# Optimization experiments

Measured on AMD Instinct MI355X. Metric: run time of the kernel, lower is better.

## Reference

```python
import jax, jax.numpy as jnp
import numpy as np

N = 20000
E = 320000
DIM_IN, DIM_H, DIM_OUT, HEADS = 500, 32, 16, 8
NEG_SLOPE = 0.2


def _glorot(key, shape, fan_in, fan_out):
    s = jnp.sqrt(6.0 / (fan_in + fan_out))
    return jax.random.uniform(key, shape, jnp.float32, -s, s)


def setup_inputs() -> dict:
    key = jax.random.key(0)
    ks = jax.random.split(key, 16)
    x = jax.random.normal(ks[0], (N, DIM_IN), jnp.float32)
    edge_index = jax.random.randint(ks[1], (2, E), 0, N, jnp.int64)
    h1 = HEADS * DIM_H   # 256
    h2 = HEADS * DIM_OUT  # 128
    return {
        "x": x,
        "edge_index": edge_index,
        # layer 1: GATv2Conv(500, 32, heads=8), concat -> 256
        "W1l": _glorot(ks[2], (h1, DIM_IN), DIM_IN, h1),
        "b1l": jnp.zeros((h1,), jnp.float32),
        "W1r": _glorot(ks[3], (h1, DIM_IN), DIM_IN, h1),
        "b1r": jnp.zeros((h1,), jnp.float32),
        "att1": _glorot(ks[4], (HEADS, DIM_H), DIM_H, 1),
        "bias1": jnp.zeros((h1,), jnp.float32),
        # layer 2: GATv2Conv(256, 16, heads=8), concat -> 128
        "W2l": _glorot(ks[5], (h2, h1), h1, h2),
        "b2l": jnp.zeros((h2,), jnp.float32),
        "W2r": _glorot(ks[6], (h2, h1), h1, h2),
        "b2r": jnp.zeros((h2,), jnp.float32),
        "att2": _glorot(ks[7], (HEADS, DIM_OUT), DIM_OUT, 1),
        "bias2": jnp.zeros((h2,), jnp.float32),
    }


def _gatv2_layer(x, Wl, bl, Wr, br, att, bias, src, dst, heads, out_ch):
    n = x.shape[0]
    xl = (x @ Wl.T + bl).reshape(n, heads, out_ch)  # source transform
    xr = (x @ Wr.T + br).reshape(n, heads, out_ch)  # target transform
    e = xl[src] + xr[dst]                            # [E', H, C]
    e = jnp.where(e >= 0, e, NEG_SLOPE * e)          # LeakyReLU(0.2)
    logits = jnp.einsum('ehc,hc->eh', e, att)        # [E', H]
    # segment softmax over incoming edges of each dst node
    m = jax.ops.segment_max(logits, dst, num_segments=n)
    ex = jnp.exp(logits - m[dst])
    denom = jax.ops.segment_sum(ex, dst, num_segments=n)
    alpha = ex / denom[dst]                          # [E', H]
    out = jax.ops.segment_sum(xl[src] * alpha[:, :, None], dst, num_segments=n)
    return out.reshape(n, heads * out_ch) + bias


def reference(x, edge_index, W1l, b1l, W1r, b1r, att1, bias1,
              W2l, b2l, W2r, b2r, att2, bias2):
    n = x.shape[0]
    loop = jnp.arange(n, dtype=edge_index.dtype)
    src = jnp.concatenate([edge_index[0], loop])  # PyG add_self_loops=True
    dst = jnp.concatenate([edge_index[1], loop])
    h = _gatv2_layer(x, W1l, b1l, W1r, b1r, att1, bias1, src, dst, HEADS, DIM_H)
    h = jax.nn.elu(h)  # normalization='none' -> Identity; eval-mode dropout is identity
    h = _gatv2_layer(h, W2l, b2l, W2r, b2r, att2, bias2, src, dst, HEADS, DIM_OUT)
    return jax.nn.log_softmax(h, axis=1)
```

## Files before the change

kernel.cpp:

```cpp
#include <hip/hip_runtime.h>
#include <math.h>

#define DIN   500
#define H1    256
#define H2    128
#define NEG_SLOPE 0.2f

typedef __attribute__((ext_vector_type(8))) short short8;
typedef __attribute__((ext_vector_type(4))) float floatx4;

static __device__ __forceinline__ unsigned short f2bf(float f) {
    union { float f; unsigned int u; } x; x.f = f;
    unsigned int r = x.u + 0x7fffu + ((x.u >> 16) & 1u);
    return (unsigned short)(r >> 16);
}
static __device__ __forceinline__ float bitsf(unsigned int i) {
    union { unsigned int i; float f; } x; x.i = i;
    return x.f;
}
static __device__ __forceinline__ void cvt8(uint4 u, float* o) {
    o[0] = bitsf(u.x << 16); o[1] = bitsf(u.x & 0xffff0000u);
    o[2] = bitsf(u.y << 16); o[3] = bitsf(u.y & 0xffff0000u);
    o[4] = bitsf(u.z << 16); o[5] = bitsf(u.z & 0xffff0000u);
    o[6] = bitsf(u.w << 16); o[7] = bitsf(u.w & 0xffff0000u);
}

template<int SHIFT>
static __device__ __forceinline__ void cast_seg(const float* __restrict__ src,
                                                unsigned short* __restrict__ dst,
                                                int M, int K, long base, long total) {
    if (base >= total) return;
    int row = (int)(base >> SHIFT);
    int c   = (int)(base & ((1 << SHIFT) - 1));
    const float* srow = src + (size_t)row * K;
    unsigned short tmp[8];
    #pragma unroll
    for (int j = 0; j < 8; ++j) {
        int cc = c + j;
        float v = (row < M && cc < K) ? srow[cc] : 0.f;
        tmp[j] = f2bf(v);
    }
    *reinterpret_cast<int4*>(dst + base) = *reinterpret_cast<const int4*>(tmp);
}

__global__ __launch_bounds__(256) void prep(const float* __restrict__ x,
                                            const float* __restrict__ W1l,
                                            const float* __restrict__ W1r,
                                            const float* __restrict__ W2l,
                                            const float* __restrict__ W2r,
                                            unsigned short* __restrict__ xb,
                                            unsigned short* __restrict__ W1b,
                                            unsigned short* __restrict__ W2b,
                                            int* __restrict__ counts,
                                            int N, int Mpad,
                                            int ZB, int XB, int W1B, int W2B) {
    int bid = blockIdx.x;
    int tid = threadIdx.x;
    if (bid < ZB) {
        int i = bid * 256 + tid;
        if (i < N) counts[i] = 1;
        else if (i == N) counts[N] = 0;
        return;
    }
    bid -= ZB;
    if (bid < XB) {
        long base = ((long)bid * 256 + tid) * 8;
        cast_seg<9>(x, xb, N, DIN, base, (long)Mpad * 512);
        return;
    }
    bid -= XB;
    if (bid < W1B) {
        long base = ((long)bid * 256 + tid) * 8;
        cast_seg<9>(W1l, W1b, H1, DIN, base, (long)H1 * 512);
        return;
    }
    bid -= W1B;
    if (bid < W1B) {
        long base = ((long)bid * 256 + tid) * 8;
        cast_seg<9>(W1r, W1b + (size_t)H1 * 512, H1, DIN, base, (long)H1 * 512);
        return;
    }
    bid -= W1B;
    if (bid < W2B) {
        long base = ((long)bid * 256 + tid) * 8;
        cast_seg<8>(W2l, W2b, H2, H1, base, (long)H2 * H1);
        return;
    }
    bid -= W2B;
    {
        long base = ((long)bid * 256 + tid) * 8;
        cast_seg<8>(W2r, W2b + (size_t)H2 * H1, H2, H1, base, (long)H2 * H1);
    }
}


__global__ void count_deg(const int* __restrict__ dst, int E, int* __restrict__ counts) {
    int i = blockIdx.x * blockDim.x + threadIdx.x;
    if (i < E) atomicAdd(&counts[dst[i]], 1);
}

__global__ __launch_bounds__(1024) void scan_all(const int* __restrict__ counts,
                                                 int* __restrict__ excl,
                                                 int* __restrict__ bsum,
                                                 int* __restrict__ done,
                                                 int* __restrict__ offsets,
                                                 int* __restrict__ cursor,
                                                 int n, int total_edges, int nb) {
    __shared__ int s[1024];
    __shared__ int sb[32];
    __shared__ int ticket;
    int tid = threadIdx.x;
    int bid = blockIdx.x;
    int i = bid * 1024 + tid;
    int v = (i < n) ? counts[i] : 0;
    s[tid] = v;
    __syncthreads();
    #pragma unroll
    for (int off = 1; off < 1024; off <<= 1) {
        int t = (tid >= off) ? s[tid - off] : 0;
        __syncthreads();
        s[tid] += t;
        __syncthreads();
    }
    if (i < n) excl[i] = s[tid] - v;
    if (tid == 1023) bsum[bid] = s[1023];
    __syncthreads();
    if (tid == 0) {
        __threadfence();
        ticket = __hip_atomic_fetch_add(done, 1, __ATOMIC_ACQ_REL, __HIP_MEMORY_SCOPE_AGENT);
    }
    __syncthreads();
    if (ticket == nb - 1) {
        __threadfence();
        if (tid == 0) {
            int run = 0;
            for (int j = 0; j < nb; ++j) { int t = bsum[j]; sb[j] = run; run += t; }
        }
        __syncthreads();
        for (int j = tid; j < n; j += 1024) {
            int o = excl[j] + sb[j >> 10];
            offsets[j] = o;
            cursor[j]  = o;
        }
        if (tid == 0) offsets[n] = total_edges;
    }
}

template<int MODE>
static __device__ __forceinline__ void gemm_body(unsigned short* lA, unsigned short* lB,
                                                 const unsigned short* __restrict__ A,
                                                 const unsigned short* __restrict__ W,
                                                 const float* __restrict__ b_lo,
                                                 const float* __restrict__ b_hi,
                                                 int halfN,
                                                 unsigned short* __restrict__ Cb,
                                                 float* __restrict__ Cf,
                                                 int M, int Nc, int K,
                                                 int bm, int bn) {
    int tid  = threadIdx.x;
    int lane = tid & 63;
    int wid  = tid >> 6;
    int wr   = wid >> 1, wc = wid & 1;

    floatx4 acc[4][4] = {};

    int st_r = (lane >> 3);
    int st_p = (lane & 7);

    for (int k0 = 0; k0 < K; k0 += 64) {
        #pragma unroll
        for (int i = 0; i < 4; ++i) {
            int r = i * 32 + wid * 8 + st_r;
            int s = st_p ^ (r & 7);
            const unsigned short* ga = A + (size_t)(bm + r) * K + k0 + s * 8;
            const unsigned short* gb = W + (size_t)(bn + r) * K + k0 + s * 8;
            __builtin_amdgcn_global_load_lds(
                (const __attribute__((address_space(1))) void*)ga,
                (__attribute__((address_space(3))) void*)((char*)lA + i * 4096 + wid * 1024),
                16, 0, 0);
            __builtin_amdgcn_global_load_lds(
                (const __attribute__((address_space(1))) void*)gb,
                (__attribute__((address_space(3))) void*)((char*)lB + i * 4096 + wid * 1024),
                16, 0, 0);
        }
        __syncthreads();

        #pragma unroll
        for (int kk = 0; kk < 2; ++kk) {
            int sbase = kk * 4 + (lane >> 4);
            short8 af[4], bf[4];
            #pragma unroll
            for (int ar = 0; ar < 4; ++ar) {
                int lr = wr * 64 + ar * 16 + (lane & 15);
                af[ar] = *reinterpret_cast<const short8*>(
                    (const char*)lA + lr * 128 + ((sbase ^ (lr & 7)) * 16));
            }
            #pragma unroll
            for (int bc = 0; bc < 4; ++bc) {
                int lc = wc * 64 + bc * 16 + (lane & 15);
                bf[bc] = *reinterpret_cast<const short8*>(
                    (const char*)lB + lc * 128 + ((sbase ^ (lc & 7)) * 16));
            }
            #pragma unroll
            for (int ar = 0; ar < 4; ++ar)
                #pragma unroll
                for (int bc = 0; bc < 4; ++bc)
                    acc[ar][bc] = __builtin_amdgcn_mfma_f32_16x16x32_bf16(
                        af[ar], bf[bc], acc[ar][bc], 0, 0, 0);
        }
        __syncthreads();
    }

    #pragma unroll
    for (int ar = 0; ar < 4; ++ar) {
        #pragma unroll
        for (int bc = 0; bc < 4; ++bc) {
            int col = bn + wc * 64 + bc * 16 + (lane & 15);
            float bv = (col < halfN) ? b_lo[col] : b_hi[col - halfN];
            #pragma unroll
            for (int r = 0; r < 4; ++r) {
                int row = bm + wr * 64 + ar * 16 + (lane >> 4) * 4 + r;
                if (row < M) {
                    float v = acc[ar][bc][r] + bv;
                    if (MODE == 1) {
                        Cb[(size_t)row * Nc + col] = f2bf(v);
                    } else {
                        if (col < halfN) Cb[(size_t)row * halfN + col] = f2bf(v);
                        else             Cf[(size_t)row * halfN + col - halfN] = v;
                    }
                }
            }
        }
    }
}

__global__ __launch_bounds__(256) void gemm1_scatter(const unsigned short* __restrict__ A,
                                                     const unsigned short* __restrict__ W,
                                                     const float* __restrict__ b_lo,
                                                     const float* __restrict__ b_hi,
                                                     unsigned short* __restrict__ Cb,
                                                     const int* __restrict__ src,
                                                     const int* __restrict__ dst,
                                                     int E, int N,
                                                     int* __restrict__ cursor,
                                                     int* __restrict__ esrc,
                                                     int GB, int M, int Nc, int K) {
    __shared__ unsigned short lA[128 * 64];
    __shared__ unsigned short lB[128 * 64];
    int bid = blockIdx.x;
    if (bid < GB) {
        gemm_body<1>(lA, lB, A, W, b_lo, b_hi, Nc >> 1, Cb, nullptr, M, Nc, K,
                     (bid >> 2) * 128, (bid & 3) * 128);
    } else {
        int i = (bid - GB) * 256 + threadIdx.x;
        int total = E + N;
        if (i < total) {
            int d, s;
            if (i < E) { d = dst[i]; s = src[i]; }
            else       { d = i - E; s = i - E; }
            int pos = atomicAdd(&cursor[d], 1);
            esrc[pos] = s;
        }
    }
}

__global__ __launch_bounds__(256) void gemm2_k(const unsigned short* __restrict__ A,
                                               const unsigned short* __restrict__ W,
                                               const float* __restrict__ b_lo,
                                               const float* __restrict__ b_hi,
                                               int halfN,
                                               unsigned short* __restrict__ Cb,
                                               float* __restrict__ Cf,
                                               int M, int Nc, int K) {
    __shared__ unsigned short lA[128 * 64];
    __shared__ unsigned short lB[128 * 64];
    gemm_body<2>(lA, lB, A, W, b_lo, b_hi, halfN, Cb, Cf, M, Nc, K,
                 blockIdx.x * 128, blockIdx.y * 128);
}

__global__ __launch_bounds__(256) void gat_edge1(const unsigned short* __restrict__ xlr,
                                                 const float* __restrict__ att,
                                                 const float* __restrict__ bias,
                                                 const int* __restrict__ offsets,
                                                 const int* __restrict__ esrc,
                                                 unsigned short* __restrict__ hb,
                                                 int N) {
    int node = blockIdx.x * 4 + (threadIdx.x >> 6);
    int lane = threadIdx.x & 63;
    int sub  = lane >> 4;
    int ln   = lane & 15;
    int c0   = ln * 16;
    if (node >= N) {
        if (sub == 0) {
            int4 z = {0, 0, 0, 0};
            int4* pp = reinterpret_cast<int4*>(&hb[(size_t)node * H1 + c0]);
            pp[0] = z; pp[1] = z;
        }
        return;
    }
    const unsigned short* xrrow = xlr + ((size_t)node << 9) + 256 + c0;
    float r_[16];
    cvt8(*reinterpret_cast<const uint4*>(xrrow),     r_);
    cvt8(*reinterpret_cast<const uint4*>(xrrow + 8), r_ + 8);
    float a_[16];
    #pragma unroll
    for (int j = 0; j < 4; ++j)
        *reinterpret_cast<float4*>(&a_[j * 4]) =
            *reinterpret_cast<const float4*>(&att[c0 + j * 4]);

    float d = 0.f;
    float ac[16];
    #pragma unroll
    for (int j = 0; j < 16; ++j) ac[j] = 0.f;

    int beg = offsets[node], end = offsets[node + 1];
    int k = beg + sub;
    bool v_c = (k < end);
    bool v_n = (k + 4 < end);
    int s_c = esrc[v_c ? k : beg];
    int s_n = esrc[v_n ? k + 4 : beg];
    const unsigned short* rc = xlr + ((size_t)s_c << 9) + c0;
    uint4 c0v = *reinterpret_cast<const uint4*>(rc);
    uint4 c1v = *reinterpret_cast<const uint4*>(rc + 8);

    while (v_c) {
        const unsigned short* rn = xlr + ((size_t)s_n << 9) + c0;
        uint4 n0v = *reinterpret_cast<const uint4*>(rn);
        uint4 n1v = *reinterpret_cast<const uint4*>(rn + 8);
        bool v_nn = (k + 8 < end);
        int s_nn = esrc[v_nn ? k + 8 : beg];

        float l_[16];
        cvt8(c0v, l_); cvt8(c1v, l_ + 8);
        float p0 = 0.f, p1 = 0.f;
        #pragma unroll
        for (int j = 0; j < 8; ++j) {
            float e0 = l_[j]     + r_[j];     e0 = fmaxf(e0, NEG_SLOPE * e0);
            float e1 = l_[j + 8] + r_[j + 8]; e1 = fmaxf(e1, NEG_SLOPE * e1);
            p0 = fmaf(e0, a_[j], p0);
            p1 = fmaf(e1, a_[j + 8], p1);
        }
        float p = p0 + p1;
        p += __shfl_xor(p, 1, 2);
        float w = __expf(p);
        d += w;
        #pragma unroll
        for (int j = 0; j < 16; ++j) ac[j] = fmaf(w, l_[j], ac[j]);

        c0v = n0v; c1v = n1v;
        s_c = s_n; s_n = s_nn;
        v_c = v_n; v_n = v_nn;
        k += 4;
    }

    #pragma unroll
    for (int off = 16; off <= 32; off <<= 1) {
        d += __shfl_xor(d, off, 64);
        #pragma unroll
        for (int j = 0; j < 16; ++j) ac[j] += __shfl_xor(ac[j], off, 64);
    }

    if (sub == 0) {
        float inv = 1.f / d;
        unsigned int ow[8];
        #pragma unroll
        for (int j = 0; j < 8; ++j) {
            float o0 = ac[2 * j]     * inv + bias[c0 + 2 * j];
            float o1 = ac[2 * j + 1] * inv + bias[c0 + 2 * j + 1];
            o0 = (o0 > 0.f) ? o0 : __expf(o0) - 1.f;
            o1 = (o1 > 0.f) ? o1 : __expf(o1) - 1.f;
            ow[j] = (unsigned int)f2bf(o0) | ((unsigned int)f2bf(o1) << 16);
        }
        uint4* pp = reinterpret_cast<uint4*>(&hb[(size_t)node * H1 + c0]);
        pp[0] = make_uint4(ow[0], ow[1], ow[2], ow[3]);
        pp[1] = make_uint4(ow[4], ow[5], ow[6], ow[7]);
    }
}

__global__ __launch_bounds__(256) void gat_edge2(const unsigned short* __restrict__ xl2b,
                                                 const float* __restrict__ xr2f,
                                                 const float* __restrict__ att,
                                                 const float* __restrict__ bias,
                                                 const int* __restrict__ offsets,
                                                 const int* __restrict__ esrc,
                                                 float* __restrict__ out,
                                                 int N) {
    int node = blockIdx.x * 4 + (threadIdx.x >> 6);
    if (node >= N) return;
    int lane = threadIdx.x & 63;
    int sub  = lane >> 4;
    int ln   = lane & 15;
    int c0   = ln * 8;

    float r_[8];
    *reinterpret_cast<float4*>(&r_[0]) =
        *reinterpret_cast<const float4*>(&xr2f[(size_t)node * H2 + c0]);
    *reinterpret_cast<float4*>(&r_[4]) =
        *reinterpret_cast<const float4*>(&xr2f[(size_t)node * H2 + c0 + 4]);
    float a_[8];
    *reinterpret_cast<float4*>(&a_[0]) = *reinterpret_cast<const float4*>(&att[c0]);
    *reinterpret_cast<float4*>(&a_[4]) = *reinterpret_cast<const float4*>(&att[c0 + 4]);

    float d = 0.f;
    float ac[8];
    #pragma unroll
    for (int j = 0; j < 8; ++j) ac[j] = 0.f;

    int beg = offsets[node], end = offsets[node + 1];
    int k = beg + sub;
    bool v_c = (k < end);
    bool v_n = (k + 4 < end);
    int s_c = esrc[v_c ? k : beg];
    int s_n = esrc[v_n ? k + 4 : beg];
    uint4 cv = *reinterpret_cast<const uint4*>(&xl2b[(size_t)s_c * H2 + c0]);

    while (v_c) {
        uint4 nv = *reinterpret_cast<const uint4*>(&xl2b[(size_t)s_n * H2 + c0]);
        bool v_nn = (k + 8 < end);
        int s_nn = esrc[v_nn ? k + 8 : beg];

        float l_[8];
        cvt8(cv, l_);
        float p0 = 0.f, p1 = 0.f;
        #pragma unroll
        for (int j = 0; j < 4; ++j) {
            float e0 = l_[j]     + r_[j];     e0 = fmaxf(e0, NEG_SLOPE * e0);
            float e1 = l_[j + 4] + r_[j + 4]; e1 = fmaxf(e1, NEG_SLOPE * e1);
            p0 = fmaf(e0, a_[j], p0);
            p1 = fmaf(e1, a_[j + 4], p1);
        }
        float p = p0 + p1;
        p += __shfl_xor(p, 1, 2);
        float w = __expf(p);
        d += w;
        #pragma unroll
        for (int j = 0; j < 8; ++j) ac[j] = fmaf(w, l_[j], ac[j]);

        cv = nv;
        s_c = s_n; s_n = s_nn;
        v_c = v_n; v_n = v_nn;
        k += 4;
    }

    #pragma unroll
    for (int off = 16; off <= 32; off <<= 1) {
        d += __shfl_xor(d, off, 64);
        #pragma unroll
        for (int j = 0; j < 8; ++j) ac[j] += __shfl_xor(ac[j], off, 64);
    }

    float inv = 1.f / d;
    float v[8];
    #pragma unroll
    for (int j = 0; j < 8; ++j) v[j] = ac[j] * inv + bias[c0 + j];
    float lm = v[0];
    #pragma unroll
    for (int j = 1; j < 8; ++j) lm = fmaxf(lm, v[j]);
    #pragma unroll
    for (int off = 1; off < 16; off <<= 1) lm = fmaxf(lm, __shfl_xor(lm, off, 16));
    float se = 0.f;
    #pragma unroll
    for (int j = 0; j < 8; ++j) se += __expf(v[j] - lm);
    #pragma unroll
    for (int off = 1; off < 16; off <<= 1) se += __shfl_xor(se, off, 16);
    float lz = lm + __logf(se);

    if (sub == 0) {
        float4 o0 = { v[0] - lz, v[1] - lz, v[2] - lz, v[3] - lz };
        float4 o1 = { v[4] - lz, v[5] - lz, v[6] - lz, v[7] - lz };
        float4* pp = reinterpret_cast<float4*>(&out[(size_t)node * H2 + c0]);
        pp[0] = o0; pp[1] = o1;
    }
}


extern "C" void kernel_launch(void* const* d_in, const int* in_sizes, int n_in,
                              void* d_out, int out_size, void* d_ws, size_t ws_size,
                              hipStream_t stream) {
    const float* x     = (const float*)d_in[0];
    const int*   ei    = (const int*)d_in[1];
    const float* W1l   = (const float*)d_in[2];
    const float* b1l   = (const float*)d_in[3];
    const float* W1r   = (const float*)d_in[4];
    const float* b1r   = (const float*)d_in[5];
    const float* att1  = (const float*)d_in[6];
    const float* bias1 = (const float*)d_in[7];
    const float* W2l   = (const float*)d_in[8];
    const float* b2l   = (const float*)d_in[9];
    const float* W2r   = (const float*)d_in[10];
    const float* b2r   = (const float*)d_in[11];
    const float* att2  = (const float*)d_in[12];
    const float* bias2 = (const float*)d_in[13];
    float* out = (float*)d_out;

    const int N  = in_sizes[0] / DIN;
    const int E  = in_sizes[1] / 2;
    const int EN = E + N;
    const int Mpad = ((N + 127) / 128) * 128;
    const int K1p  = 512;
    const int* srcIdx = ei;
    const int* dstIdx = ei + E;

    char* ws = (char*)d_ws;
    unsigned short* xb   = (unsigned short*)ws; ws += (size_t)Mpad * K1p * sizeof(short);
    unsigned short* W1b  = (unsigned short*)ws; ws += (size_t)(2 * H1) * K1p * sizeof(short);
    unsigned short* W2b  = (unsigned short*)ws; ws += (size_t)(2 * H2) * H1 * sizeof(short);
    unsigned short* xlr1 = (unsigned short*)ws; ws += (size_t)Mpad * (2 * H1) * sizeof(short);
    unsigned short* hb   = (unsigned short*)ws; ws += (size_t)Mpad * H1 * sizeof(short);
    unsigned short* xl2b = (unsigned short*)ws; ws += (size_t)Mpad * H2 * sizeof(short);
    float* xr2f = (float*)ws; ws += (size_t)Mpad * H2 * sizeof(float);
    int* counts  = (int*)ws;  ws += (size_t)(N + 1) * sizeof(int);
    int* excl    = (int*)ws;  ws += (size_t)N * sizeof(int);
    int* bsum    = (int*)ws;  ws += 64 * sizeof(int);
    int* offsets = (int*)ws;  ws += (size_t)(N + 1) * sizeof(int);
    int* cursor  = (int*)ws;  ws += (size_t)N * sizeof(int);
    int* esrc    = (int*)ws;  ws += (size_t)EN * sizeof(int);

    const int ZB  = (N + 1 + 255) / 256;
    const int XB  = (int)(((long)Mpad * K1p / 8 + 255) / 256);
    const int W1B = (H1 * K1p / 8 + 255) / 256;
    const int W2B = (H2 * H1 / 8 + 255) / 256;
    const int nb  = (N + 1023) / 1024;

    prep<<<ZB + XB + 2 * W1B + 2 * W2B, 256, 0, stream>>>(
        x, W1l, W1r, W2l, W2r, xb, W1b, W2b, counts, N, Mpad, ZB, XB, W1B, W2B);

    count_deg<<<(E + 255) / 256, 256, 0, stream>>>(dstIdx, E, counts);

    scan_all<<<nb, 1024, 0, stream>>>(counts, excl, bsum, counts + N,
                                      offsets, cursor, N, EN, nb);

    const int GB = (Mpad / 128) * ((2 * H1) / 128);
    const int SB = (EN + 255) / 256;
    gemm1_scatter<<<GB + SB, 256, 0, stream>>>(xb, W1b, b1l, b1r, xlr1,
                                               srcIdx, dstIdx, E, N, cursor, esrc,
                                               GB, Mpad, 2 * H1, K1p);

    gat_edge1<<<Mpad / 4, 256, 0, stream>>>(xlr1, att1, bias1, offsets, esrc, hb, N);

    gemm2_k<<<dim3(Mpad / 128, (2 * H2) / 128), 256, 0, stream>>>(
        hb, W2b, b2l, b2r, H2, xl2b, xr2f, N, 2 * H2, H1);

    gat_edge2<<<(N + 3) / 4, 256, 0, stream>>>(xl2b, xr2f, att2, bias2, offsets, esrc, out, N);
}
```

Baseline: 152.8 us.

## Double-buffer GEMM LDS loads, swizzle blocks across XCDs, fuse degree count with scan

The GEMM main loop now double-buffers its LDS tiles, issuing the next k-tile's global-to-LDS loads before computing the current tile, with explicit vmcnt waits and raw barriers. Both GEMM kernels remap block ids with an XCD-aware swizzle so neighbouring tiles land on the same chiplet and share L2. The separate degree-count and scan kernels are merged into one launch in which the last-arriving block performs a 256-thread chunked scan. This doubles LDS per block, which may cut occupancy, and the single-block serial scan may become a tail bottleneck.

```diff
diff --git a/kernel.cpp b/kernel.cpp
--- a/kernel.cpp
+++ b/kernel.cpp
@@ -23,6 +23,11 @@
     o[2] = bitsf(u.y << 16); o[3] = bitsf(u.y & 0xffff0000u);
     o[4] = bitsf(u.z << 16); o[5] = bitsf(u.z & 0xffff0000u);
     o[6] = bitsf(u.w << 16); o[7] = bitsf(u.w & 0xffff0000u);
+}
+static __device__ __forceinline__ int xcd_swz(int bid, int nwg) {
+    int q = nwg >> 3, r = nwg & 7;
+    int x = bid & 7, idx = bid >> 3;
+    return (x < r ? x * (q + 1) : r * (q + 1) + (x - r) * q) + idx;
 }
 
 template<int SHIFT>
@@ -93,57 +98,45 @@
     }
 }
 
-
-__global__ void count_deg(const int* __restrict__ dst, int E, int* __restrict__ counts) {
-    int i = blockIdx.x * blockDim.x + threadIdx.x;
+__global__ __launch_bounds__(256) void count_scan(const int* __restrict__ dst,
+                                                  int E, int N, int EN,
+                                                  int* __restrict__ counts,
+                                                  int* __restrict__ done,
+                                                  int* __restrict__ offsets,
+                                                  int* __restrict__ cursor, int CB) {
+    int i = blockIdx.x * 256 + threadIdx.x;
     if (i < E) atomicAdd(&counts[dst[i]], 1);
-}
-
-__global__ __launch_bounds__(1024) void scan_all(const int* __restrict__ counts,
-                                                 int* __restrict__ excl,
-                                                 int* __restrict__ bsum,
-                                                 int* __restrict__ done,
-                                                 int* __restrict__ offsets,
-                                                 int* __restrict__ cursor,
-                                                 int n, int total_edges, int nb) {
-    __shared__ int s[1024];
-    __shared__ int sb[32];
+    __syncthreads();
     __shared__ int ticket;
-    int tid = threadIdx.x;
-    int bid = blockIdx.x;
-    int i = bid * 1024 + tid;
-    int v = (i < n) ? counts[i] : 0;
-    s[tid] = v;
-    __syncthreads();
-    #pragma unroll
-    for (int off = 1; off < 1024; off <<= 1) {
-        int t = (tid >= off) ? s[tid - off] : 0;
-        __syncthreads();
-        s[tid] += t;
-        __syncthreads();
-    }
-    if (i < n) excl[i] = s[tid] - v;
-    if (tid == 1023) bsum[bid] = s[1023];
-    __syncthreads();
-    if (tid == 0) {
+    if (threadIdx.x == 0) {
         __threadfence();
         ticket = __hip_atomic_fetch_add(done, 1, __ATOMIC_ACQ_REL, __HIP_MEMORY_SCOPE_AGENT);
     }
     __syncthreads();
-    if (ticket == nb - 1) {
-        __threadfence();
-        if (tid == 0) {
-            int run = 0;
-            for (int j = 0; j < nb; ++j) { int t = bsum[j]; sb[j] = run; run += t; }
-        }
+    if (ticket != CB - 1) return;
+    __threadfence();
+    __shared__ int part[256];
+    int tid = threadIdx.x;
+    int per = (N + 255) >> 8;
+    int lo = tid * per;
+    int hi = lo + per; if (hi > N) hi = N;
+    int sum = 0;
+    for (int j = lo; j < hi; ++j) sum += counts[j];
+    part[tid] = sum;
+    __syncthreads();
+    #pragma unroll
+    for (int off = 1; off < 256; off <<= 1) {
+        int t = (tid >= off) ? part[tid - off] : 0;
         __syncthreads();
-        for (int j = tid; j < n; j += 1024) {
-            int o = excl[j] + sb[j >> 10];
-            offsets[j] = o;
-            cursor[j]  = o;
-        }
-        if (tid == 0) offsets[n] = total_edges;
-    }
+        part[tid] += t;
+        __syncthreads();
+    }
+    int run = part[tid] - sum;
+    for (int j = lo; j < hi; ++j) {
+        int c = counts[j];
+        offsets[j] = run; cursor[j] = run; run += c;
+    }
+    if (tid == 255) offsets[N] = EN;
 }
 
 template<int MODE>
@@ -167,24 +160,39 @@
     int st_r = (lane >> 3);
     int st_p = (lane & 7);
 
-    for (int k0 = 0; k0 < K; k0 += 64) {
-        #pragma unroll
-        for (int i = 0; i < 4; ++i) {
-            int r = i * 32 + wid * 8 + st_r;
-            int s = st_p ^ (r & 7);
-            const unsigned short* ga = A + (size_t)(bm + r) * K + k0 + s * 8;
-            const unsigned short* gb = W + (size_t)(bn + r) * K + k0 + s * 8;
-            __builtin_amdgcn_global_load_lds(
-                (const __attribute__((address_space(1))) void*)ga,
-                (__attribute__((address_space(3))) void*)((char*)lA + i * 4096 + wid * 1024),
-                16, 0, 0);
-            __builtin_amdgcn_global_load_lds(
-                (const __attribute__((address_space(1))) void*)gb,
-                (__attribute__((address_space(3))) void*)((char*)lB + i * 4096 + wid * 1024),
-                16, 0, 0);
-        }
-        __syncthreads();
-
+    #define STAGE(BUF, K0) do {                                                             \
+        _Pragma("unroll")                                                                   \
+        for (int i_ = 0; i_ < 4; ++i_) {                                                    \
+            int r_ = i_ * 32 + wid * 8 + st_r;                                              \
+            int s_ = st_p ^ (r_ & 7);                                                       \
+            const unsigned short* ga_ = A + (size_t)(bm + r_) * K + (K0) + s_ * 8;          \
+            const unsigned short* gb_ = W + (size_t)(bn + r_) * K + (K0) + s_ * 8;          \
+            __builtin_amdgcn_global_load_lds(                                               \
+                (const __attribute__((address_space(1))) void*)ga_,                         \
+                (__attribute__((address_space(3))) void*)((char*)lA + (BUF) * 16384 + i_ * 4096 + wid * 1024), \
+                16, 0, 0);                                                                  \
+            __builtin_amdgcn_global_load_lds(                                               \
+                (const __attribute__((address_space(1))) void*)gb_,                         \
+                (__attribute__((address_space(3))) void*)((char*)lB + (BUF) * 16384 + i_ * 4096 + wid * 1024), \
+                16, 0, 0);                                                                  \
+        } } while (0)
+
+    const int nt = K >> 6;
+    STAGE(0, 0);
+    int cur = 0;
+    for (int t = 0; t < nt; ++t) {
+        if (t + 1 < nt) {
+            STAGE(cur ^ 1, (t + 1) << 6);
+            asm volatile("s_waitcnt vmcnt(8)" ::: "memory");
+        } else {
+            asm volatile("s_waitcnt vmcnt(0)" ::: "memory");
+        }
+        __builtin_amdgcn_sched_barrier(0);
+        __builtin_amdgcn_s_barrier();
+        __builtin_amdgcn_sched_barrier(0);
+
+        const char* bA = (const char*)lA + cur * 16384;
+        const char* bB = (const char*)lB + cur * 16384;
         #pragma unroll
         for (int kk = 0; kk < 2; ++kk) {
             int sbase = kk * 4 + (lane >> 4);
@@ -192,14 +200,12 @@
             #pragma unroll
             for (int ar = 0; ar < 4; ++ar) {
                 int lr = wr * 64 + ar * 16 + (lane & 15);
-                af[ar] = *reinterpret_cast<const short8*>(
-                    (const char*)lA + lr * 128 + ((sbase ^ (lr & 7)) * 16));
+                af[ar] = *reinterpret_cast<const short8*>(bA + lr * 128 + ((sbase ^ (lr & 7)) * 16));
             }
             #pragma unroll
             for (int bc = 0; bc < 4; ++bc) {
                 int lc = wc * 64 + bc * 16 + (lane & 15);
-                bf[bc] = *reinterpret_cast<const short8*>(
-                    (const char*)lB + lc * 128 + ((sbase ^ (lc & 7)) * 16));
+                bf[bc] = *reinterpret_cast<const short8*>(bB + lc * 128 + ((sbase ^ (lc & 7)) * 16));
             }
             #pragma unroll
             for (int ar = 0; ar < 4; ++ar)
@@ -208,8 +214,11 @@
                     acc[ar][bc] = __builtin_amdgcn_mfma_f32_16x16x32_bf16(
                         af[ar], bf[bc], acc[ar][bc], 0, 0, 0);
         }
-        __syncthreads();
-    }
+        __builtin_amdgcn_sched_barrier(0);
+        __builtin_amdgcn_s_barrier();
+        cur ^= 1;
+    }
+    #undef STAGE
 
     #pragma unroll
     for (int ar = 0; ar < 4; ++ar) {
@@ -245,12 +254,13 @@
                                                      int* __restrict__ cursor,
                                                      int* __restrict__ esrc,
                                                      int GB, int M, int Nc, int K) {
-    __shared__ unsigned short lA[128 * 64];
-    __shared__ unsigned short lB[128 * 64];
+    __shared__ unsigned short lA[2 * 128 * 64];
+    __shared__ unsigned short lB[2 * 128 * 64];
     int bid = blockIdx.x;
     if (bid < GB) {
+        int lg = xcd_swz(bid, GB);
         gemm_body<1>(lA, lB, A, W, b_lo, b_hi, Nc >> 1, Cb, nullptr, M, Nc, K,
-                     (bid >> 2) * 128, (bid & 3) * 128);
+                     (lg >> 2) * 128, (lg & 3) * 128);
     } else {
         int i = (bid - GB) * 256 + threadIdx.x;
         int total = E + N;
@@ -271,11 +281,12 @@
                                                int halfN,
                                                unsigned short* __restrict__ Cb,
                                                float* __restrict__ Cf,
-                                               int M, int Nc, int K) {
-    __shared__ unsigned short lA[128 * 64];
-    __shared__ unsigned short lB[128 * 64];
+                                               int nwg, int M, int Nc, int K) {
+    __shared__ unsigned short lA[2 * 128 * 64];
+    __shared__ unsigned short lB[2 * 128 * 64];
+    int lg = xcd_swz(blockIdx.x, nwg);
     gemm_body<2>(lA, lB, A, W, b_lo, b_hi, halfN, Cb, Cf, M, Nc, K,
-                 blockIdx.x * 128, blockIdx.y * 128);
+                 (lg >> 1) * 128, (lg & 1) * 128);
 }
 
 __global__ __launch_bounds__(256) void gat_edge1(const unsigned short* __restrict__ xlr,
@@ -510,8 +521,6 @@
     unsigned short* xl2b = (unsigned short*)ws; ws += (size_t)Mpad * H2 * sizeof(short);
     float* xr2f = (float*)ws; ws += (size_t)Mpad * H2 * sizeof(float);
     int* counts  = (int*)ws;  ws += (size_t)(N + 1) * sizeof(int);
-    int* excl    = (int*)ws;  ws += (size_t)N * sizeof(int);
-    int* bsum    = (int*)ws;  ws += 64 * sizeof(int);
     int* offsets = (int*)ws;  ws += (size_t)(N + 1) * sizeof(int);
     int* cursor  = (int*)ws;  ws += (size_t)N * sizeof(int);
     int* esrc    = (int*)ws;  ws += (size_t)EN * sizeof(int);
@@ -520,15 +529,13 @@
     const int XB  = (int)(((long)Mpad * K1p / 8 + 255) / 256);
     const int W1B = (H1 * K1p / 8 + 255) / 256;
     const int W2B = (H2 * H1 / 8 + 255) / 256;
-    const int nb  = (N + 1023) / 1024;
 
     prep<<<ZB + XB + 2 * W1B + 2 * W2B, 256, 0, stream>>>(
         x, W1l, W1r, W2l, W2r, xb, W1b, W2b, counts, N, Mpad, ZB, XB, W1B, W2B);
 
-    count_deg<<<(E + 255) / 256, 256, 0, stream>>>(dstIdx, E, counts);
-
-    scan_all<<<nb, 1024, 0, stream>>>(counts, excl, bsum, counts + N,
-                                      offsets, cursor, N, EN, nb);
+    const int CB = (E + 255) / 256;
+    count_scan<<<CB, 256, 0, stream>>>(dstIdx, E, N, EN, counts, counts + N,
+                                       offsets, cursor, CB);
 
     const int GB = (Mpad / 128) * ((2 * H1) / 128);
     const int SB = (EN + 255) / 256;
@@ -538,8 +545,8 @@
 
     gat_edge1<<<Mpad / 4, 256, 0, stream>>>(xlr1, att1, bias1, offsets, esrc, hb, N);
 
-    gemm2_k<<<dim3(Mpad / 128, (2 * H2) / 128), 256, 0, stream>>>(
-        hb, W2b, b2l, b2r, H2, xl2b, xr2f, N, 2 * H2, H1);
+    const int G2 = (Mpad / 128) * ((2 * H2) / 128);
+    gemm2_k<<<G2, 256, 0, stream>>>(hb, W2b, b2l, b2r, H2, xl2b, xr2f, G2, N, 2 * H2, H1);
 
     gat_edge2<<<(N + 3) / 4, 256, 0, stream>>>(xl2b, xr2f, att2, bias2, offsets, esrc, out, N);
 }
```

Result: slower. 231.9 us (+51.8%).
